# Kernel optimization log

Measured on AMD Instinct MI355X. Metric: run time of the kernel, lower is better.

Reference implementation:

```python
import jax, jax.numpy as jnp
import numpy as np

H = 12  # max_heads

def setup_inputs() -> dict:
    key = jax.random.key(0)
    ks = jax.random.split(key, 5)
    B, N, E = 8, 1024, 768
    return {
        "x": jax.random.normal(ks[0], (B, N, E), dtype=jnp.float32),
        "w_qkv": jax.random.normal(ks[1], (3 * E, E), dtype=jnp.float32) * 0.02,
        "b_qkv": jax.random.normal(ks[2], (3 * E,), dtype=jnp.float32) * 0.02,
        "w_proj": jax.random.normal(ks[3], (E, E), dtype=jnp.float32) * 0.02,
        "b_proj": jax.random.normal(ks[4], (E,), dtype=jnp.float32) * 0.02,
        "active_heads": 8,
    }

def reference(x, w_qkv, b_qkv, w_proj, b_proj, active_heads):
    B, N, E = x.shape
    D = E // H
    scale = D ** -0.5
    # qkv projection: [B,N,3E] -> [3,B,H,N,D]
    qkv = (x @ w_qkv.T + b_qkv).reshape(B, N, 3, H, D)
    qkv = jnp.transpose(qkv, (2, 0, 3, 1, 4))
    q, k, v = qkv[0], qkv[1], qkv[2]
    # head mask from active_heads (static int)
    head_mask = (jnp.arange(H) < active_heads).astype(x.dtype)
    m = head_mask[None, :, None, None]
    q = q * m
    k = k * m
    v = v * m
    attn = jax.nn.softmax(jnp.einsum("bhqd,bhkd->bhqk", q, k) * scale, axis=-1)
    out = jnp.einsum("bhqk,bhkd->bhqd", attn, v)
    out = jnp.transpose(out, (0, 2, 1, 3)).reshape(B, N, E)
    channel_mask = jnp.repeat(head_mask, D)  # [E]
    out = out * channel_mask[None, None, :]
    return out @ w_proj.T + b_proj
```

## Files before the change

kernel.cpp:

```cpp
#include <hip/hip_runtime.h>
#include <hip/hip_fp16.h>

#define NH 12
#define BSZ 8
#define NSEQ 1024
#define EDIM 768
#define DH 64

typedef _Float16 f16;
typedef f16 half8 __attribute__((ext_vector_type(8)));
typedef f16 half4 __attribute__((ext_vector_type(4)));
typedef float f32x4 __attribute__((ext_vector_type(4)));
typedef unsigned int u32;
typedef u32 u32x2 __attribute__((ext_vector_type(2)));

static __device__ __forceinline__ void gload16(const void* g, void* l) {
    __builtin_amdgcn_global_load_lds((const __attribute__((address_space(1))) u32*)g,
                                     (__attribute__((address_space(3))) u32*)l, 16, 0, 0);
}
static __device__ __forceinline__ u32 pkrtz(float a, float b) {
    auto h = __builtin_amdgcn_cvt_pkrtz(a, b);
    return __builtin_bit_cast(u32, h);
}
#define MFMA16(a, b, c) __builtin_amdgcn_mfma_f32_16x16x32_f16((a), (b), (c), 0, 0, 0)

__global__ void cvt_all_kernel(const float* __restrict__ x, const float* __restrict__ wq,
                               const float* __restrict__ wp, f16* __restrict__ dst) {
    const int NX = BSZ * NSEQ * EDIM;
    const int NWQ = 3 * EDIM * EDIM;
    int i = (blockIdx.x * blockDim.x + threadIdx.x) * 4;
    const float* s;
    int j;
    if (i < NX) { s = x; j = i; }
    else if (i < NX + NWQ) { s = wq; j = i - NX; }
    else { s = wp; j = i - NX - NWQ; }
    float4 v = *(const float4*)(s + j);
    half4 o = { (f16)v.x, (f16)v.y, (f16)v.z, (f16)v.w };
    *(half4*)(dst + i) = o;
}

template<int MODE>
__global__ __launch_bounds__(256) void gemm_kernel(
    const f16* __restrict__ A, const f16* __restrict__ Wt, const float* __restrict__ bias,
    f16* __restrict__ qbuf, f16* __restrict__ kbuf, f16* __restrict__ vtbuf,
    float* __restrict__ outp, const int* __restrict__ activep, int Kd, int NCd)
{
    constexpr int K = EDIM;
    constexpr int NKT = K / 32;
    constexpr int NB = (MODE == 0) ? 18 : 6;
    constexpr int SMSZ = (MODE == 0) ? 34816 : 32768;

    __shared__ __align__(16) char smem[SMSZ];
    f16 (*Ah)[2][4][64][8] = (f16 (*)[2][4][64][8])smem;
    f16 (*Bh)[2][4][64][8] = (f16 (*)[2][4][64][8])(smem + 16384);

    const int lin = blockIdx.x;
    const int xcd = lin & 7, pos = lin >> 3;
    const int bx = pos % NB;
    const int my = xcd + (pos / NB) * 8;
    const int c0 = bx * 128;
    const int m0 = my * 128;
    const int ah = *activep;
    if (MODE == 0) {
        if (((c0 % EDIM) >> 6) >= ah) return;
    }
    const int nkt = (MODE == 1) ? (2 * ah) : NKT;
    const int tid = threadIdx.x;
    const int lane = tid & 63;
    const int wid  = tid >> 6;
    const int wr = wid >> 1;
    const int wc = wid & 1;
    const int r16 = lane & 15, rg = lane >> 4;

    f32x4 acc[4][4];
#pragma unroll
    for (int i = 0; i < 4; ++i)
#pragma unroll
        for (int j = 0; j < 4; ++j)
            acc[i][j] = f32x4{0.f, 0.f, 0.f, 0.f};

    const int s0 = 2 * wid, s1 = 2 * wid + 1;
    const f16* gA0 = A  + (size_t)(m0 + (s0 >> 2) * 64 + (s0 & 3) * 16 + r16) * K + rg * 8;
    const f16* gA1 = A  + (size_t)(m0 + (s1 >> 2) * 64 + (s1 & 3) * 16 + r16) * K + rg * 8;
    const f16* gB0 = Wt + (size_t)(c0 + (s0 >> 2) * 64 + (s0 & 3) * 16 + r16) * K + rg * 8;
    const f16* gB1 = Wt + (size_t)(c0 + (s1 >> 2) * 64 + (s1 & 3) * 16 + r16) * K + rg * 8;

    auto stage = [&](int buf, int kt) {
        gload16(gA0 + kt * 32, &Ah[buf][s0 >> 2][s0 & 3][0][0]);
        gload16(gA1 + kt * 32, &Ah[buf][s1 >> 2][s1 & 3][0][0]);
        gload16(gB0 + kt * 32, &Bh[buf][s0 >> 2][s0 & 3][0][0]);
        gload16(gB1 + kt * 32, &Bh[buf][s1 >> 2][s1 & 3][0][0]);
    };

    if (nkt > 0) stage(0, 0);
    if (nkt > 1) stage(1, 1);
    asm volatile("s_waitcnt vmcnt(4)" ::: "memory");
    __builtin_amdgcn_s_barrier();
    __builtin_amdgcn_sched_barrier(0);

#pragma unroll 1
    for (int kt = 0; kt < nkt; ++kt) {
        const int cur = kt & 1;
        half8 af[4], bf[4];
#pragma unroll
        for (int f = 0; f < 4; ++f) {
            af[f] = *(const half8*)&Ah[cur][wr][f][lane][0];
            bf[f] = *(const half8*)&Bh[cur][wc][f][lane][0];
        }
        asm volatile("s_waitcnt lgkmcnt(0)" ::: "memory");
        __builtin_amdgcn_sched_barrier(0);
        __builtin_amdgcn_s_barrier();
        __builtin_amdgcn_sched_barrier(0);
        if (kt + 2 < nkt) stage(cur, kt + 2);
        __builtin_amdgcn_sched_barrier(0);
        __builtin_amdgcn_s_setprio(1);
#pragma unroll
        for (int fm = 0; fm < 4; ++fm)
#pragma unroll
            for (int fn = 0; fn < 4; ++fn)
                acc[fm][fn] = MFMA16(af[fm], bf[fn], acc[fm][fn]);
        __builtin_amdgcn_s_setprio(0);
        if (kt + 1 < nkt) {
            if (kt + 2 < nkt) asm volatile("s_waitcnt vmcnt(4)" ::: "memory");
            else              asm volatile("s_waitcnt vmcnt(0)" ::: "memory");
            __builtin_amdgcn_s_barrier();
            __builtin_amdgcn_sched_barrier(0);
        }
    }

    if (MODE == 0 && c0 >= 2 * EDIM) {
        f16 (*T)[136] = (f16 (*)[136])smem;
        __syncthreads();
#pragma unroll
        for (int fn = 0; fn < 4; ++fn) {
            const int cl = wc * 64 + fn * 16 + r16;
            const float bv = bias[c0 + cl];
#pragma unroll
            for (int fm = 0; fm < 4; ++fm) {
                const int ml = wr * 64 + fm * 16 + rg * 4;
                half4 o = { (f16)(acc[fm][fn][0] + bv), (f16)(acc[fm][fn][1] + bv),
                            (f16)(acc[fm][fn][2] + bv), (f16)(acc[fm][fn][3] + bv) };
                *(half4*)&T[cl][ml] = o;
            }
        }
        __syncthreads();
        const int cc0 = c0 - 2 * EDIM;
        const int bb = m0 >> 10, n0 = m0 & 1023;
        const int row = tid >> 1, hsel = tid & 1;
        const int hh = (cc0 + row) >> 6;
        if (hh < ah) {
            f16* dst = vtbuf + (((size_t)bb * NH + hh) * DH + ((cc0 + row) & 63)) * NSEQ
                     + n0 + hsel * 64;
#pragma unroll
            for (int j = 0; j < 8; ++j)
                *(half8*)(dst + j * 8) = *(const half8*)&T[row][hsel * 64 + j * 8];
        }
        return;
    }

#pragma unroll
    for (int fn = 0; fn < 4; ++fn) {
        const int c = c0 + wc * 64 + fn * 16 + r16;
        const float bv = bias[c];
        const bool colActive = (MODE == 1) || (((c % EDIM) >> 6) < ah);
#pragma unroll
        for (int fm = 0; fm < 4; ++fm) {
            const int mbase = m0 + wr * 64 + fm * 16 + rg * 4;
#pragma unroll
            for (int r = 0; r < 4; ++r) {
                const float val = acc[fm][fn][r] + bv;
                const int m = mbase + r;
                if (MODE == 1) {
                    outp[(size_t)m * EDIM + c] = val;
                } else if (colActive) {
                    const int s  = c / EDIM;
                    const int cc = c % EDIM;
                    const int hh = cc >> 6, d = cc & 63;
                    const int bb = m >> 10, n = m & 1023;
                    f16* dst = (s == 0) ? qbuf : kbuf;
                    dst[(((size_t)bb * NH + hh) * NSEQ + n) * DH + d] = (f16)val;
                }
            }
        }
    }
}

__global__ __launch_bounds__(512) void attn_kernel(
    const f16* __restrict__ qbuf, const f16* __restrict__ kbuf, const f16* __restrict__ vtb,
    f16* __restrict__ ctx, const int* __restrict__ activep)
{
    __shared__ __align__(16) f16 Kh[2][2][64][64];
    __shared__ __align__(16) f16 Vh[2][2][64][64];
    __shared__ __align__(16) f16 Ph[8][16][64];

    const int b = blockIdx.z, h = blockIdx.y;
    const int q0 = blockIdx.x * 128;
    const int tid = threadIdx.x, lane = tid & 63, wid = tid >> 6;

    if (h >= *activep) return;

    const size_t hb = (((size_t)b * NH + h) * NSEQ) * DH;
    const f16* Q  = qbuf + hb;
    const char* Kp = (const char*)(kbuf + hb);
    const char* Vp = (const char*)(vtb + hb);

    const int ql = lane & 15;
    const int g  = lane >> 4;
    const int q7 = ql & 7;

    half8 qb0, qb1;
    {
        const f16 qsc = (f16)0.18033688f;
        const f16* qp = Q + (size_t)(q0 + wid * 16 + ql) * DH + g * 8;
        qb0 = *(const half8*)qp        * qsc;
        qb1 = *(const half8*)(qp + 32) * qsc;
    }
    const half8 ones = { (f16)1, (f16)1, (f16)1, (f16)1, (f16)1, (f16)1, (f16)1, (f16)1 };

    const int srow8 = lane >> 3;
    const int schk  = (lane & 7) ^ srow8;
    const int qh4   = wid & 3;

    auto stage = [&](int buf, int pp) {
#pragma unroll
        for (int hf = 0; hf < 2; ++hf) {
            const int kt = 2 * pp + hf;
            if (wid < 4) {
                const char* kb = Kp + (size_t)kt * 8192;
#pragma unroll
                for (int i = 0; i < 2; ++i) {
                    const int r = qh4 * 16 + i * 8 + srow8;
                    gload16(kb + (size_t)r * 128 + schk * 16, &Kh[buf][hf][qh4 * 16 + i * 8][0]);
                }
            } else {
#pragma unroll
                for (int i = 0; i < 2; ++i) {
                    const int r = qh4 * 16 + i * 8 + srow8;
                    gload16(Vp + (size_t)r * (NSEQ * 2) + (size_t)kt * 128 + schk * 16,
                            &Vh[buf][hf][qh4 * 16 + i * 8][0]);
                }
            }
        }
    };

    f32x4 oacc[4];
#pragma unroll
    for (int i = 0; i < 4; ++i) oacc[i] = f32x4{0.f, 0.f, 0.f, 0.f};
    f32x4 lacc = f32x4{0.f, 0.f, 0.f, 0.f};

    char* prow = (char*)&Ph[wid][ql][0];

    stage(0, 0);
    const int NP = NSEQ / 128;
#pragma unroll 1
    for (int pp = 0; pp < NP; ++pp) {
        const int cur = pp & 1;
        __syncthreads();
        if (pp + 1 < NP) stage(cur ^ 1, pp + 1);

        f32x4 st[2][4];
        __builtin_amdgcn_s_setprio(1);
#pragma unroll
        for (int hf = 0; hf < 2; ++hf)
#pragma unroll
            for (int s = 0; s < 4; ++s) {
                f32x4 t = f32x4{0.f, 0.f, 0.f, 0.f};
                t = MFMA16(*(const half8*)((const char*)&Kh[cur][hf][16 * s + ql][0] + ((g ^ q7) << 4)),       qb0, t);
                t = MFMA16(*(const half8*)((const char*)&Kh[cur][hf][16 * s + ql][0] + (((4 | g) ^ q7) << 4)), qb1, t);
                st[hf][s] = t;
            }
        __builtin_amdgcn_s_setprio(0);

#pragma unroll
        for (int hf = 0; hf < 2; ++hf)
#pragma unroll
            for (int s = 0; s < 4; ++s)
#pragma unroll
                for (int r = 0; r < 4; ++r)
                    st[hf][s][r] = exp2f(st[hf][s][r]);

#pragma unroll
        for (int hf = 0; hf < 2; ++hf) {
#pragma unroll
            for (int s = 0; s < 4; ++s) {
                u32x2 w = { pkrtz(st[hf][s][0], st[hf][s][1]), pkrtz(st[hf][s][2], st[hf][s][3]) };
                *(u32x2*)(prow + ((32 * s + 8 * g) ^ (q7 << 4))) = w;
            }
            const half8 pa0 = *(const half8*)(prow + ((16 * g) ^ (q7 << 4)));
            const half8 pa1 = *(const half8*)(prow + ((64 + 16 * g) ^ (q7 << 4)));

            __builtin_amdgcn_s_setprio(1);
            lacc = MFMA16(pa0, ones, lacc);
            lacc = MFMA16(pa1, ones, lacc);
#pragma unroll
            for (int db = 0; db < 4; ++db) {
                oacc[db] = MFMA16(pa0, *(const half8*)((const char*)&Vh[cur][hf][16 * db + ql][0] + ((g ^ q7) << 4)),       oacc[db]);
                oacc[db] = MFMA16(pa1, *(const half8*)((const char*)&Vh[cur][hf][16 * db + ql][0] + (((4 | g) ^ q7) << 4)), oacc[db]);
            }
            __builtin_amdgcn_s_setprio(0);
        }
    }

#pragma unroll
    for (int r = 0; r < 4; ++r) {
        const float li = 1.0f / lacc[r];
        const int n = q0 + wid * 16 + (g << 2) + r;
#pragma unroll
        for (int db = 0; db < 4; ++db)
            ctx[((size_t)b * NSEQ + n) * EDIM + h * DH + db * 16 + ql] = (f16)(oacc[db][r] * li);
    }
}

extern "C" void kernel_launch(void* const* d_in, const int* in_sizes, int n_in,
                              void* d_out, int out_size, void* d_ws, size_t ws_size,
                              hipStream_t stream) {
    const float* x      = (const float*)d_in[0];
    const float* w_qkv  = (const float*)d_in[1];
    const float* b_qkv  = (const float*)d_in[2];
    const float* w_proj = (const float*)d_in[3];
    const float* b_proj = (const float*)d_in[4];
    const int*   active = (const int*)d_in[5];
    float* out = (float*)d_out;

    char* ws = (char*)d_ws;
    const size_t n_x  = (size_t)BSZ * NSEQ * EDIM;
    const size_t n_wq = (size_t)3 * EDIM * EDIM;
    const size_t n_wp = (size_t)EDIM * EDIM;
    const size_t n_hd = (size_t)BSZ * NH * NSEQ * DH;

    f16* xh   = (f16*)ws;
    f16* wqh  = xh + n_x;
    f16* wph  = wqh + n_wq;
    f16* qh   = wph + n_wp;
    f16* kh   = qh + n_hd;
    f16* vtb  = kh + n_hd;
    f16* ctxh = vtb + n_hd;

    const size_t n_cvt = n_x + n_wq + n_wp;
    cvt_all_kernel<<<(int)(n_cvt / 4 / 256), 256, 0, stream>>>(x, w_qkv, w_proj, xh);

    gemm_kernel<0><<<dim3(64 * 18), 256, 0, stream>>>(
        xh, wqh, b_qkv, qh, kh, vtb, nullptr, active, EDIM, 3 * EDIM);

    attn_kernel<<<dim3(NSEQ / 128, NH, BSZ), 512, 0, stream>>>(qh, kh, vtb, ctxh, active);

    gemm_kernel<1><<<dim3(64 * 6), 256, 0, stream>>>(
        ctxh, wph, b_proj, nullptr, nullptr, nullptr, out, active, EDIM, EDIM);
}
```

Measured before the change: 109.9 us.

## Fuse fp32-to-fp16 conversion of x into QKV GEMM A-tile loading

Drops the separate conversion pass over the activation tensor x. The QKV GEMM now reads fp32 x straight into registers, packs it to fp16 with cvt_pkrtz and writes it to LDS, while weights are still staged with global_load_lds. The goal is to avoid writing and re-reading a 12 MB fp16 copy of x. The cost is that each GEMM block reads twice as many bytes for A, the same rows are reread by many column blocks, and the pipeline now needs register staging plus extra barriers.

After: 133.7 us. +21.7%, slower.

```diff
diff --git a/kernel.cpp b/kernel.cpp
--- a/kernel.cpp
+++ b/kernel.cpp
@@ -13,6 +13,7 @@
 typedef float f32x4 __attribute__((ext_vector_type(4)));
 typedef unsigned int u32;
 typedef u32 u32x2 __attribute__((ext_vector_type(2)));
+typedef u32 u32x4 __attribute__((ext_vector_type(4)));
 
 static __device__ __forceinline__ void gload16(const void* g, void* l) {
     __builtin_amdgcn_global_load_lds((const __attribute__((address_space(1))) u32*)g,
@@ -24,16 +25,14 @@
 }
 #define MFMA16(a, b, c) __builtin_amdgcn_mfma_f32_16x16x32_f16((a), (b), (c), 0, 0, 0)
 
-__global__ void cvt_all_kernel(const float* __restrict__ x, const float* __restrict__ wq,
-                               const float* __restrict__ wp, f16* __restrict__ dst) {
-    const int NX = BSZ * NSEQ * EDIM;
+__global__ void cvt_w_kernel(const float* __restrict__ wq, const float* __restrict__ wp,
+                             f16* __restrict__ dst) {
     const int NWQ = 3 * EDIM * EDIM;
     int i = (blockIdx.x * blockDim.x + threadIdx.x) * 4;
     const float* s;
     int j;
-    if (i < NX) { s = x; j = i; }
-    else if (i < NX + NWQ) { s = wq; j = i - NX; }
-    else { s = wp; j = i - NX - NWQ; }
+    if (i < NWQ) { s = wq; j = i; }
+    else { s = wp; j = i - NWQ; }
     float4 v = *(const float4*)(s + j);
     half4 o = { (f16)v.x, (f16)v.y, (f16)v.z, (f16)v.w };
     *(half4*)(dst + i) = o;
@@ -41,9 +40,10 @@
 
 template<int MODE>
 __global__ __launch_bounds__(256) void gemm_kernel(
-    const f16* __restrict__ A, const f16* __restrict__ Wt, const float* __restrict__ bias,
+    const float* __restrict__ Axf, const f16* __restrict__ A16,
+    const f16* __restrict__ Wt, const float* __restrict__ bias,
     f16* __restrict__ qbuf, f16* __restrict__ kbuf, f16* __restrict__ vtbuf,
-    float* __restrict__ outp, const int* __restrict__ activep, int Kd, int NCd)
+    float* __restrict__ outp, const int* __restrict__ activep)
 {
     constexpr int K = EDIM;
     constexpr int NKT = K / 32;
@@ -64,7 +64,6 @@
     if (MODE == 0) {
         if (((c0 % EDIM) >> 6) >= ah) return;
     }
-    const int nkt = (MODE == 1) ? (2 * ah) : NKT;
     const int tid = threadIdx.x;
     const int lane = tid & 63;
     const int wid  = tid >> 6;
@@ -80,51 +79,139 @@
             acc[i][j] = f32x4{0.f, 0.f, 0.f, 0.f};
 
     const int s0 = 2 * wid, s1 = 2 * wid + 1;
-    const f16* gA0 = A  + (size_t)(m0 + (s0 >> 2) * 64 + (s0 & 3) * 16 + r16) * K + rg * 8;
-    const f16* gA1 = A  + (size_t)(m0 + (s1 >> 2) * 64 + (s1 & 3) * 16 + r16) * K + rg * 8;
+    const int rowA0 = m0 + (s0 >> 2) * 64 + (s0 & 3) * 16 + r16;
+    const int rowA1 = m0 + (s1 >> 2) * 64 + (s1 & 3) * 16 + r16;
     const f16* gB0 = Wt + (size_t)(c0 + (s0 >> 2) * 64 + (s0 & 3) * 16 + r16) * K + rg * 8;
     const f16* gB1 = Wt + (size_t)(c0 + (s1 >> 2) * 64 + (s1 & 3) * 16 + r16) * K + rg * 8;
 
-    auto stage = [&](int buf, int kt) {
-        gload16(gA0 + kt * 32, &Ah[buf][s0 >> 2][s0 & 3][0][0]);
-        gload16(gA1 + kt * 32, &Ah[buf][s1 >> 2][s1 & 3][0][0]);
-        gload16(gB0 + kt * 32, &Bh[buf][s0 >> 2][s0 & 3][0][0]);
-        gload16(gB1 + kt * 32, &Bh[buf][s1 >> 2][s1 & 3][0][0]);
-    };
-
-    if (nkt > 0) stage(0, 0);
-    if (nkt > 1) stage(1, 1);
-    asm volatile("s_waitcnt vmcnt(4)" ::: "memory");
-    __builtin_amdgcn_s_barrier();
-    __builtin_amdgcn_sched_barrier(0);
-
-#pragma unroll 1
-    for (int kt = 0; kt < nkt; ++kt) {
-        const int cur = kt & 1;
-        half8 af[4], bf[4];
-#pragma unroll
-        for (int f = 0; f < 4; ++f) {
-            af[f] = *(const half8*)&Ah[cur][wr][f][lane][0];
-            bf[f] = *(const half8*)&Bh[cur][wc][f][lane][0];
-        }
+#define BST(buf, kt)                                                     \
+    gload16(gB0 + (kt) * 32, &Bh[buf][s0 >> 2][s0 & 3][0][0]);           \
+    gload16(gB1 + (kt) * 32, &Bh[buf][s1 >> 2][s1 & 3][0][0]);
+
+#define FRAGS(buf)                                                       \
+    _Pragma("unroll")                                                    \
+    for (int f = 0; f < 4; ++f) {                                        \
+        af[f] = *(const half8*)&Ah[buf][wr][f][lane][0];                 \
+        bf[f] = *(const half8*)&Bh[buf][wc][f][lane][0];                 \
+    }
+
+#define DOMFMA()                                                         \
+    __builtin_amdgcn_s_setprio(1);                                       \
+    _Pragma("unroll")                                                    \
+    for (int fm = 0; fm < 4; ++fm)                                       \
+        _Pragma("unroll")                                                \
+        for (int fn = 0; fn < 4; ++fn)                                   \
+            acc[fm][fn] = MFMA16(af[fm], bf[fn], acc[fm][fn]);           \
+    __builtin_amdgcn_s_setprio(0);
+
+    if constexpr (MODE == 0) {
+        const float* gAx0 = Axf + (size_t)rowA0 * K + rg * 8;
+        const float* gAx1 = Axf + (size_t)rowA1 * K + rg * 8;
+
+        float4 e0lo, e0hi, e1lo, e1hi;
+        float4 o0lo, o0hi, o1lo, o1hi;
+
+#define ALOADE(kt) { e0lo = *(const float4*)(gAx0 + (kt) * 32);          \
+                     e0hi = *(const float4*)(gAx0 + (kt) * 32 + 4);      \
+                     e1lo = *(const float4*)(gAx1 + (kt) * 32);          \
+                     e1hi = *(const float4*)(gAx1 + (kt) * 32 + 4); }
+#define ALOADO(kt) { o0lo = *(const float4*)(gAx0 + (kt) * 32);          \
+                     o0hi = *(const float4*)(gAx0 + (kt) * 32 + 4);      \
+                     o1lo = *(const float4*)(gAx1 + (kt) * 32);          \
+                     o1hi = *(const float4*)(gAx1 + (kt) * 32 + 4); }
+#define AWRITEE(buf) { u32x4 w0 = { pkrtz(e0lo.x, e0lo.y), pkrtz(e0lo.z, e0lo.w),   \
+                                    pkrtz(e0hi.x, e0hi.y), pkrtz(e0hi.z, e0hi.w) }; \
+                       u32x4 w1 = { pkrtz(e1lo.x, e1lo.y), pkrtz(e1lo.z, e1lo.w),   \
+                                    pkrtz(e1hi.x, e1hi.y), pkrtz(e1hi.z, e1hi.w) }; \
+                       *(u32x4*)&Ah[buf][s0 >> 2][s0 & 3][lane][0] = w0;            \
+                       *(u32x4*)&Ah[buf][s1 >> 2][s1 & 3][lane][0] = w1; }
+#define AWRITEO(buf) { u32x4 w0 = { pkrtz(o0lo.x, o0lo.y), pkrtz(o0lo.z, o0lo.w),   \
+                                    pkrtz(o0hi.x, o0hi.y), pkrtz(o0hi.z, o0hi.w) }; \
+                       u32x4 w1 = { pkrtz(o1lo.x, o1lo.y), pkrtz(o1lo.z, o1lo.w),   \
+                                    pkrtz(o1hi.x, o1hi.y), pkrtz(o1hi.z, o1hi.w) }; \
+                       *(u32x4*)&Ah[buf][s0 >> 2][s0 & 3][lane][0] = w0;            \
+                       *(u32x4*)&Ah[buf][s1 >> 2][s1 & 3][lane][0] = w1; }
+
+        ALOADE(0); BST(0, 0);
+        ALOADO(1); BST(1, 1);
+        AWRITEE(0);
+        asm volatile("s_waitcnt vmcnt(6)" ::: "memory");
         asm volatile("s_waitcnt lgkmcnt(0)" ::: "memory");
-        __builtin_amdgcn_sched_barrier(0);
         __builtin_amdgcn_s_barrier();
         __builtin_amdgcn_sched_barrier(0);
-        if (kt + 2 < nkt) stage(cur, kt + 2);
+
+        half8 af[4], bf[4];
+#pragma unroll 1
+        for (int t = 0; t < NKT; t += 2) {
+            FRAGS(0)
+            asm volatile("s_waitcnt lgkmcnt(0)" ::: "memory");
+            __builtin_amdgcn_sched_barrier(0);
+            __builtin_amdgcn_s_barrier();
+            __builtin_amdgcn_sched_barrier(0);
+            if (t + 2 < NKT) { ALOADE(t + 2); BST(0, t + 2); }
+            __builtin_amdgcn_sched_barrier(0);
+            DOMFMA()
+            AWRITEO(1);
+            if (t + 2 < NKT) asm volatile("s_waitcnt vmcnt(6)" ::: "memory");
+            else             asm volatile("s_waitcnt vmcnt(0)" ::: "memory");
+            asm volatile("s_waitcnt lgkmcnt(0)" ::: "memory");
+            __builtin_amdgcn_sched_barrier(0);
+            __builtin_amdgcn_s_barrier();
+            __builtin_amdgcn_sched_barrier(0);
+
+            FRAGS(1)
+            asm volatile("s_waitcnt lgkmcnt(0)" ::: "memory");
+            __builtin_amdgcn_sched_barrier(0);
+            __builtin_amdgcn_s_barrier();
+            __builtin_amdgcn_sched_barrier(0);
+            if (t + 3 < NKT) { ALOADO(t + 3); BST(1, t + 3); }
+            __builtin_amdgcn_sched_barrier(0);
+            DOMFMA()
+            if (t + 2 < NKT) {
+                AWRITEE(0);
+                if (t + 3 < NKT) asm volatile("s_waitcnt vmcnt(6)" ::: "memory");
+                else             asm volatile("s_waitcnt vmcnt(0)" ::: "memory");
+                asm volatile("s_waitcnt lgkmcnt(0)" ::: "memory");
+                __builtin_amdgcn_sched_barrier(0);
+                __builtin_amdgcn_s_barrier();
+                __builtin_amdgcn_sched_barrier(0);
+            }
+        }
+    } else {
+        const int nkt = 2 * ah;
+        const f16* gA0 = A16 + (size_t)rowA0 * K + rg * 8;
+        const f16* gA1 = A16 + (size_t)rowA1 * K + rg * 8;
+
+        auto stage = [&](int buf, int kt) {
+            gload16(gA0 + kt * 32, &Ah[buf][s0 >> 2][s0 & 3][0][0]);
+            gload16(gA1 + kt * 32, &Ah[buf][s1 >> 2][s1 & 3][0][0]);
+            BST(buf, kt)
+        };
+
+        if (nkt > 0) stage(0, 0);
+        if (nkt > 1) stage(1, 1);
+        asm volatile("s_waitcnt vmcnt(4)" ::: "memory");
+        __builtin_amdgcn_s_barrier();
         __builtin_amdgcn_sched_barrier(0);
-        __builtin_amdgcn_s_setprio(1);
-#pragma unroll
-        for (int fm = 0; fm < 4; ++fm)
-#pragma unroll
-            for (int fn = 0; fn < 4; ++fn)
-                acc[fm][fn] = MFMA16(af[fm], bf[fn], acc[fm][fn]);
-        __builtin_amdgcn_s_setprio(0);
-        if (kt + 1 < nkt) {
-            if (kt + 2 < nkt) asm volatile("s_waitcnt vmcnt(4)" ::: "memory");
-            else              asm volatile("s_waitcnt vmcnt(0)" ::: "memory");
+
+#pragma unroll 1
+        for (int kt = 0; kt < nkt; ++kt) {
+            const int cur = kt & 1;
+            half8 af[4], bf[4];
+            FRAGS(cur)
+            asm volatile("s_waitcnt lgkmcnt(0)" ::: "memory");
+            __builtin_amdgcn_sched_barrier(0);
             __builtin_amdgcn_s_barrier();
             __builtin_amdgcn_sched_barrier(0);
+            if (kt + 2 < nkt) stage(cur, kt + 2);
+            __builtin_amdgcn_sched_barrier(0);
+            DOMFMA()
+            if (kt + 1 < nkt) {
+                if (kt + 2 < nkt) asm volatile("s_waitcnt vmcnt(4)" ::: "memory");
+                else              asm volatile("s_waitcnt vmcnt(0)" ::: "memory");
+                __builtin_amdgcn_s_barrier();
+                __builtin_amdgcn_sched_barrier(0);
+            }
         }
     }
 
@@ -323,27 +410,25 @@
     float* out = (float*)d_out;
 
     char* ws = (char*)d_ws;
-    const size_t n_x  = (size_t)BSZ * NSEQ * EDIM;
     const size_t n_wq = (size_t)3 * EDIM * EDIM;
     const size_t n_wp = (size_t)EDIM * EDIM;
     const size_t n_hd = (size_t)BSZ * NH * NSEQ * DH;
 
-    f16* xh   = (f16*)ws;
-    f16* wqh  = xh + n_x;
+    f16* wqh  = (f16*)ws;
     f16* wph  = wqh + n_wq;
     f16* qh   = wph + n_wp;
     f16* kh   = qh + n_hd;
     f16* vtb  = kh + n_hd;
     f16* ctxh = vtb + n_hd;
 
-    const size_t n_cvt = n_x + n_wq + n_wp;
-    cvt_all_kernel<<<(int)(n_cvt / 4 / 256), 256, 0, stream>>>(x, w_qkv, w_proj, xh);
+    const size_t n_cvt = n_wq + n_wp;
+    cvt_w_kernel<<<(int)(n_cvt / 4 / 256), 256, 0, stream>>>(w_qkv, w_proj, wqh);
 
     gemm_kernel<0><<<dim3(64 * 18), 256, 0, stream>>>(
-        xh, wqh, b_qkv, qh, kh, vtb, nullptr, active, EDIM, 3 * EDIM);
+        x, nullptr, wqh, b_qkv, qh, kh, vtb, nullptr, active);
 
     attn_kernel<<<dim3(NSEQ / 128, NH, BSZ), 512, 0, stream>>>(qh, kh, vtb, ctxh, active);
 
     gemm_kernel<1><<<dim3(64 * 6), 256, 0, stream>>>(
-        ctxh, wph, b_proj, nullptr, nullptr, nullptr, out, active, EDIM, EDIM);
-}
+        nullptr, ctxh, wph, b_proj, nullptr, nullptr, nullptr, out, active);
+}
```
